# Kernel tuning notes

Hardware: AMD Instinct MI355X
Metric: run time of the kernel (lower is better)

Reference implementation:

```python
import jax, jax.numpy as jnp
import numpy as np
import math

D_MODEL = 768
N_HEADS = 12
D_HEAD = D_MODEL // N_HEADS


def setup_inputs() -> dict:
    key = jax.random.key(0)
    ks = jax.random.split(key, 5)
    x = jax.random.normal(ks[0], (2, 4096, D_MODEL), dtype=jnp.float32)
    s = 1.0 / math.sqrt(D_MODEL)
    W_qkv = jax.random.normal(ks[1], (D_MODEL, 3 * D_MODEL), dtype=jnp.float32) * s
    b_qkv = jnp.zeros((3 * D_MODEL,), dtype=jnp.float32)
    W_out = jax.random.normal(ks[2], (D_MODEL, D_MODEL), dtype=jnp.float32) * s
    b_out = jnp.zeros((D_MODEL,), dtype=jnp.float32)
    return {"x": x, "W_qkv": W_qkv, "b_qkv": b_qkv, "W_out": W_out, "b_out": b_out}


def reference(x, W_qkv, b_qkv, W_out, b_out):
    B, T, C = x.shape
    H, Dh = N_HEADS, D_HEAD
    qkv = x @ W_qkv + b_qkv                      # [B,T,3C]
    q, k, v = jnp.split(qkv, 3, axis=-1)
    q = q.reshape(B, T, H, Dh).transpose(0, 2, 1, 3)  # [B,H,T,Dh]
    k = k.reshape(B, T, H, Dh).transpose(0, 2, 1, 3)
    v = v.reshape(B, T, H, Dh).transpose(0, 2, 1, 3)
    att = jnp.einsum('bhqd,bhkd->bhqk', q, k) * (1.0 / math.sqrt(Dh))
    causal = jnp.tril(jnp.ones((T, T), dtype=bool))
    att = jnp.where(causal, att, -jnp.inf)
    att = jax.nn.softmax(att, axis=-1)
    out = jnp.einsum('bhqk,bhkd->bhqd', att, v)  # [B,H,T,Dh]
    out = out.transpose(0, 2, 1, 3).reshape(B, T, C)
    return out @ W_out + b_out
```

## Files before the change

### kernel.cpp

```cpp
#include <hip/hip_runtime.h>
#include <hip/hip_bf16.h>
#include <cstdint>

#define NH 12
#define DH 64
#define TSEQ 4096
#define BATCH 2
#define CDIM 768
#define MROWS (BATCH*TSEQ)

typedef __bf16 bf16x8 __attribute__((ext_vector_type(8)));
typedef __bf16 bf16x4 __attribute__((ext_vector_type(4)));
typedef bf16x8 bf16x8_a __attribute__((may_alias));
typedef bf16x4 bf16x4_a __attribute__((may_alias));
typedef float f32x4 __attribute__((ext_vector_type(4)));

__device__ __forceinline__ uint16_t f2bu(float f) {
  uint32_t u = __float_as_uint(f);
  u += 0x7fffu + ((u >> 16) & 1u);
  return (uint16_t)(u >> 16);
}

__device__ __forceinline__ float bu2f(uint16_t x) {
  return __uint_as_float(((uint32_t)x) << 16);
}

__device__ __forceinline__ void gload_lds16(const void* g, void* l) {
  __builtin_amdgcn_global_load_lds(
      (const __attribute__((address_space(1))) void*)g,
      (__attribute__((address_space(3))) void*)l, 16, 0, 0);
}

__global__ void cast_f32_bf16(const float* __restrict__ in, uint16_t* __restrict__ out, int n4) {
  int i = blockIdx.x * blockDim.x + threadIdx.x;
  int stride = gridDim.x * blockDim.x;
  for (; i < n4; i += stride) {
    float4 v = ((const float4*)in)[i];
    ushort4 o;
    o.x = f2bu(v.x); o.y = f2bu(v.y); o.z = f2bu(v.z); o.w = f2bu(v.w);
    ((ushort4*)out)[i] = o;
  }
}

__global__ void transpose_cast(const float* __restrict__ w, uint16_t* __restrict__ wt, int K, int N) {
  __shared__ float tile[32][33];
  int kb = blockIdx.x * 32, nb = blockIdx.y * 32;
  int tx = threadIdx.x & 31, ty = threadIdx.x >> 5;
  #pragma unroll
  for (int r = ty; r < 32; r += 8) tile[r][tx] = w[(size_t)(kb + r) * N + nb + tx];
  __syncthreads();
  #pragma unroll
  for (int r = ty; r < 32; r += 8) wt[(size_t)(nb + r) * K + kb + tx] = f2bu(tile[tx][r]);
}

template <int MODE>
__global__ __launch_bounds__(256) void gemm_bt(
    const uint16_t* __restrict__ A, const uint16_t* __restrict__ Bt,
    const float* __restrict__ bias,
    uint16_t* __restrict__ q, uint16_t* __restrict__ k, uint16_t* __restrict__ v,
    float* __restrict__ outf, int N, int K) {
  __shared__ uint16_t As[128 * 32];
  __shared__ uint16_t Bs[128 * 32];
  int tid = threadIdx.x;
  int w = tid >> 6, l = tid & 63;
  int lg = l >> 4, lr = l & 15;
  int mb = blockIdx.x * 128, nb = blockIdx.y * 128;
  int wr = (w >> 1) * 64, wc = (w & 1) * 64;
  f32x4 acc[4][4] = {};
  int srow = tid >> 2, scol = (tid & 3) * 8;
  const uint16_t* Ag = A + (size_t)(mb + srow) * K + scol;
  const uint16_t* Bg = Bt + (size_t)(nb + srow) * K + scol;
  char* AsB = (char*)As + (size_t)w * 1024;
  char* BsB = (char*)Bs + (size_t)w * 1024;
  size_t rowskip = (size_t)64 * K;
  for (int kb = 0; kb < K; kb += 32) {
    __syncthreads();
    gload_lds16(Ag + kb, AsB);
    gload_lds16(Ag + kb + rowskip, AsB + 4096);
    gload_lds16(Bg + kb, BsB);
    gload_lds16(Bg + kb + rowskip, BsB + 4096);
    __syncthreads();
    bf16x8 af[4], bfr[4];
    #pragma unroll
    for (int i = 0; i < 4; ++i)
      af[i] = *(const bf16x8_a*)(const void*)(As + (wr + i * 16 + lr) * 32 + lg * 8);
    #pragma unroll
    for (int i = 0; i < 4; ++i)
      bfr[i] = *(const bf16x8_a*)(const void*)(Bs + (wc + i * 16 + lr) * 32 + lg * 8);
    #pragma unroll
    for (int mi = 0; mi < 4; ++mi)
      #pragma unroll
      for (int ni = 0; ni < 4; ++ni)
        acc[mi][ni] = __builtin_amdgcn_mfma_f32_16x16x32_bf16(af[mi], bfr[ni], acc[mi][ni], 0, 0, 0);
  }
  #pragma unroll
  for (int mi = 0; mi < 4; ++mi) {
    #pragma unroll
    for (int ni = 0; ni < 4; ++ni) {
      if (MODE == 0) {
        int gm0 = mb + wr + mi * 16 + lg * 4;
        int gn = nb + wc + ni * 16 + lr;
        int which = gn / CDIM;
        int cc = gn - which * CDIM;
        int hh = cc >> 6, d = cc & 63;
        float bs = bias[gn];
        if (which == 2) {
          int b0 = gm0 >> 12, t0 = gm0 & 4095;
          ushort4 pk;
          pk.x = f2bu(acc[mi][ni][0] + bs);
          pk.y = f2bu(acc[mi][ni][1] + bs);
          pk.z = f2bu(acc[mi][ni][2] + bs);
          pk.w = f2bu(acc[mi][ni][3] + bs);
          *(ushort4*)&v[(((size_t)(b0 * NH + hh)) * DH + d) * TSEQ + t0] = pk;
        } else {
          uint16_t* dst = which ? k : q;
          float sc = which ? 1.0f : 0.1803368801111204f;
          #pragma unroll
          for (int j = 0; j < 4; ++j) {
            int gm = gm0 + j;
            int bb = gm >> 12, t = gm & 4095;
            float val = (acc[mi][ni][j] + bs) * sc;
            dst[(((size_t)(bb * NH + hh)) * TSEQ + t) * DH + d] = f2bu(val);
          }
        }
      } else {
        #pragma unroll
        for (int j = 0; j < 4; ++j) {
          int gm = mb + wr + mi * 16 + lg * 4 + j;
          int gn = nb + wc + ni * 16 + lr;
          outf[(size_t)gm * N + gn] = acc[mi][ni][j] + bias[gn];
        }
      }
    }
  }
}

__device__ __forceinline__ void tile_step(
    const uint16_t* __restrict__ Kc, const uint16_t* __restrict__ Vc, char* pw,
    bf16x8 qf0, bf16x8 qf1, f32x4 (&oacc)[4], float& lsum,
    bool diag, int thr, int lg, int lr, int swzA, int swzB) {
  f32x4 sacc[4];
  __builtin_amdgcn_s_setprio(1);
  #pragma unroll
  for (int ni = 0; ni < 4; ++ni) {
    const char* kb = (const char*)Kc + (ni * 16 + lr) * 128;
    bf16x8 kf0 = *(const bf16x8_a*)(kb + swzA);
    bf16x8 kf1 = *(const bf16x8_a*)(kb + swzB);
    f32x4 s = {};
    s = __builtin_amdgcn_mfma_f32_16x16x32_bf16(kf0, qf0, s, 0, 0, 0);
    s = __builtin_amdgcn_mfma_f32_16x16x32_bf16(kf1, qf1, s, 0, 0, 0);
    sacc[ni] = s;
  }
  __builtin_amdgcn_s_setprio(0);
  if (diag) {
    #pragma unroll
    for (int ni = 0; ni < 4; ++ni)
      #pragma unroll
      for (int j = 0; j < 4; ++j)
        sacc[ni][j] = (16 * ni + j <= thr) ? sacc[ni][j] : -1e30f;
  }
  int pofs = (lg & 1) * 8;
  #pragma unroll
  for (int ni = 0; ni < 4; ++ni) {
    float p0 = __builtin_amdgcn_exp2f(sacc[ni][0]);
    float p1 = __builtin_amdgcn_exp2f(sacc[ni][1]);
    float p2 = __builtin_amdgcn_exp2f(sacc[ni][2]);
    float p3 = __builtin_amdgcn_exp2f(sacc[ni][3]);
    lsum += (p0 + p1) + (p2 + p3);
    bf16x4 pk;
    pk[0] = (__bf16)p0; pk[1] = (__bf16)p1; pk[2] = (__bf16)p2; pk[3] = (__bf16)p3;
    int chunk = (2 * ni + (lg >> 1)) ^ (lr & 7);
    *(bf16x4_a*)(pw + lr * 128 + chunk * 16 + pofs) = pk;
  }
  bf16x8 pf0 = *(const bf16x8_a*)(pw + lr * 128 + swzA);
  bf16x8 pf1 = *(const bf16x8_a*)(pw + lr * 128 + swzB);
  __builtin_amdgcn_s_setprio(1);
  #pragma unroll
  for (int nd = 0; nd < 4; ++nd) {
    const char* vb = (const char*)Vc + (nd * 16 + lr) * 128;
    bf16x8 vf0 = *(const bf16x8_a*)(vb + swzA);
    bf16x8 vf1 = *(const bf16x8_a*)(vb + swzB);
    oacc[nd] = __builtin_amdgcn_mfma_f32_16x16x32_bf16(pf0, vf0, oacc[nd], 0, 0, 0);
    oacc[nd] = __builtin_amdgcn_mfma_f32_16x16x32_bf16(pf1, vf1, oacc[nd], 0, 0, 0);
  }
  __builtin_amdgcn_s_setprio(0);
}

__global__ __launch_bounds__(256) void attn_part(
    const uint16_t* __restrict__ Q, const uint16_t* __restrict__ K,
    const uint16_t* __restrict__ Vt, uint16_t* __restrict__ O,
    uint16_t* __restrict__ Pbuf, float* __restrict__ Plsum) {
  int gid = blockIdx.x;
  int widx = gid / 24, bh = gid - widx * 24;
  int qt, t0, t1, chunk;
  bool direct;
  if (widx < 32) {
    qt = 31 - (widx >> 1); chunk = widx & 1; direct = false;
    t0 = chunk ? (qt + 1) : 0;
    t1 = chunk ? (2 * qt + 1) : qt;
  } else {
    qt = 47 - widx; chunk = 0; direct = true;
    t0 = 0; t1 = 2 * qt + 1;
  }
  int b = bh / NH, hd = bh - b * NH;
  size_t base = (size_t)bh * TSEQ * DH;
  int tid = threadIdx.x, w = tid >> 6, lane = tid & 63;
  int lg = lane >> 4, lr = lane & 15;
  __shared__ uint16_t Ks[64 * 64];
  __shared__ uint16_t Vs[64 * 64];
  __shared__ uint16_t Ps[4][16 * 64];
  char* pw = (char*)Ps[w];
  int srow = tid >> 3;
  int schunk = (tid & 7) ^ (srow & 7);
  const uint16_t* Kg0 = K + base + (size_t)srow * DH + schunk * 8;
  const uint16_t* Vg0 = Vt + base + (size_t)srow * TSEQ + schunk * 8;
  char* KsB = (char*)Ks + w * 1024;
  char* VsB = (char*)Vs + w * 1024;
  int swzA = (lg ^ (lr & 7)) << 4;
  int swzB = swzA ^ 64;

  int qb = qt * 128;
  int qgA = qb + w * 16 + lr;
  int qgB = qgA + 64;
  bf16x8 qA0 = *(const bf16x8_a*)(const void*)(Q + base + (size_t)qgA * DH + lg * 8);
  bf16x8 qA1 = *(const bf16x8_a*)(const void*)(Q + base + (size_t)qgA * DH + 32 + lg * 8);
  bf16x8 qB0 = *(const bf16x8_a*)(const void*)(Q + base + (size_t)qgB * DH + lg * 8);
  bf16x8 qB1 = *(const bf16x8_a*)(const void*)(Q + base + (size_t)qgB * DH + 32 + lg * 8);
  f32x4 oA[4] = {}, oB[4] = {};
  float lA = 0.f, lB = 0.f;
  int lg4 = lg * 4;

  for (int t = t0; t <= t1; ++t) {
    __syncthreads();
    gload_lds16(Kg0 + (size_t)t * (64 * DH), KsB);
    gload_lds16(Kg0 + (size_t)t * (64 * DH) + 32 * DH, KsB + 4096);
    gload_lds16(Vg0 + (size_t)t * 64, VsB);
    gload_lds16(Vg0 + (size_t)t * 64 + (size_t)32 * TSEQ, VsB + 4096);
    __syncthreads();
    int kb0 = t * 64;
    if (t <= 2 * qt)
      tile_step(Ks, Vs, pw, qA0, qA1, oA, lA, t == 2 * qt, qgA - kb0 - lg4, lg, lr, swzA, swzB);
    tile_step(Ks, Vs, pw, qB0, qB1, oB, lB, t == 2 * qt + 1, qgB - kb0 - lg4, lg, lr, swzA, swzB);
  }

  lA += __shfl_xor(lA, 16, 64); lA += __shfl_xor(lA, 32, 64);
  lB += __shfl_xor(lB, 16, 64); lB += __shfl_xor(lB, 32, 64);
  if (direct) {
    float riA = 1.0f / lA, riB = 1.0f / lB;
    #pragma unroll
    for (int j = 0; j < 4; ++j) {
      float rvA = __shfl(riA, (lane & 48) | (lg4 + j), 64);
      float rvB = __shfl(riB, (lane & 48) | (lg4 + j), 64);
      int tA = qb + w * 16 + lg4 + j;
      size_t pA = (size_t)(b * TSEQ + tA) * CDIM + hd * DH + lr;
      size_t pB = pA + (size_t)64 * CDIM;
      #pragma unroll
      for (int nd = 0; nd < 4; ++nd) {
        O[pA + nd * 16] = f2bu(oA[nd][j] * rvA);
        O[pB + nd * 16] = f2bu(oB[nd][j] * rvB);
      }
    }
  } else {
    int pidx = (bh << 4) + (qt - 16);
    uint16_t* Pb = Pbuf + ((size_t)pidx * 2 + chunk) * 8192;
    float* Pl = Plsum + ((size_t)pidx * 2 + chunk) * 128;
    #pragma unroll
    for (int j = 0; j < 4; ++j) {
      int qlA = w * 16 + lg4 + j;
      #pragma unroll
      for (int nd = 0; nd < 4; ++nd) {
        Pb[qlA * 64 + nd * 16 + lr] = f2bu(oA[nd][j]);
        Pb[(64 + qlA) * 64 + nd * 16 + lr] = f2bu(oB[nd][j]);
      }
    }
    if (lane < 16) {
      Pl[w * 16 + lane] = lA;
      Pl[64 + w * 16 + lane] = lB;
    }
  }
}

__global__ __launch_bounds__(256) void attn_reduce(
    const uint16_t* __restrict__ Pbuf, const float* __restrict__ Plsum,
    uint16_t* __restrict__ O) {
  int pidx = blockIdx.x;
  int bh = pidx >> 4, qrel = pidx & 15;
  int qt = 16 + qrel;
  int b = bh / NH, hd = bh - b * NH;
  int d = threadIdx.x & 63, qo = threadIdx.x >> 6;
  const uint16_t* p0 = Pbuf + (size_t)pidx * 2 * 8192;
  const uint16_t* p1 = p0 + 8192;
  const float* l0 = Plsum + (size_t)pidx * 2 * 128;
  const float* l1 = l0 + 128;
  #pragma unroll 4
  for (int q = qo; q < 128; q += 4) {
    float li = 1.0f / (l0[q] + l1[q]);
    float s = bu2f(p0[q * 64 + d]) + bu2f(p1[q * 64 + d]);
    int t = qt * 128 + q;
    O[(size_t)(b * TSEQ + t) * CDIM + hd * DH + d] = f2bu(s * li);
  }
}

extern "C" void kernel_launch(void* const* d_in, const int* in_sizes, int n_in,
                              void* d_out, int out_size, void* d_ws, size_t ws_size,
                              hipStream_t stream) {
  const float* x    = (const float*)d_in[0];
  const float* Wqkv = (const float*)d_in[1];
  const float* bqkv = (const float*)d_in[2];
  const float* Wout = (const float*)d_in[3];
  const float* bout = (const float*)d_in[4];
  float* out = (float*)d_out;
  char* ws = (char*)d_ws;

  uint16_t* Xb    = (uint16_t*)(ws + 0);
  uint16_t* Wqkvt = (uint16_t*)(ws + 12582912);
  uint16_t* Woutt = (uint16_t*)(ws + 16121856);
  uint16_t* Qb    = (uint16_t*)(ws + 17301504);
  uint16_t* Kb    = (uint16_t*)(ws + 29884416);
  uint16_t* Vtb   = (uint16_t*)(ws + 42467328);
  uint16_t* Ob    = (uint16_t*)(ws + 55050240);
  uint16_t* Pbuf  = Xb;
  float*    Plsum = (float*)Wqkvt;

  cast_f32_bf16<<<2048, 256, 0, stream>>>(x, Xb, (MROWS * CDIM) / 4);
  transpose_cast<<<dim3(24, 72), 256, 0, stream>>>(Wqkv, Wqkvt, 768, 2304);
  transpose_cast<<<dim3(24, 24), 256, 0, stream>>>(Wout, Woutt, 768, 768);
  gemm_bt<0><<<dim3(64, 18), 256, 0, stream>>>(Xb, Wqkvt, bqkv, Qb, Kb, Vtb, nullptr, 2304, 768);
  attn_part<<<1152, 256, 0, stream>>>(Qb, Kb, Vtb, Ob, Pbuf, Plsum);
  attn_reduce<<<384, 256, 0, stream>>>(Pbuf, Plsum, Ob);
  gemm_bt<1><<<dim3(64, 6), 256, 0, stream>>>(Ob, Woutt, bout, nullptr, nullptr, nullptr, out, 768, 768);
}
```

Before: 196.9 us.

## Double-buffer K/V tiles and interleave both query blocks per tile

Allocates two LDS buffers for K and V and prefetches the next key tile while computing the current one, removing one barrier per iteration. It also fuses the two query-block tile steps so each K and V fragment read from LDS feeds MFMAs for both blocks. This doubles K/V LDS usage, raises register pressure, and depends on the async loads being complete by the single barrier.

```diff
diff --git a/kernel.cpp b/kernel.cpp
--- a/kernel.cpp
+++ b/kernel.cpp
@@ -135,57 +135,6 @@
   }
 }
 
-__device__ __forceinline__ void tile_step(
-    const uint16_t* __restrict__ Kc, const uint16_t* __restrict__ Vc, char* pw,
-    bf16x8 qf0, bf16x8 qf1, f32x4 (&oacc)[4], float& lsum,
-    bool diag, int thr, int lg, int lr, int swzA, int swzB) {
-  f32x4 sacc[4];
-  __builtin_amdgcn_s_setprio(1);
-  #pragma unroll
-  for (int ni = 0; ni < 4; ++ni) {
-    const char* kb = (const char*)Kc + (ni * 16 + lr) * 128;
-    bf16x8 kf0 = *(const bf16x8_a*)(kb + swzA);
-    bf16x8 kf1 = *(const bf16x8_a*)(kb + swzB);
-    f32x4 s = {};
-    s = __builtin_amdgcn_mfma_f32_16x16x32_bf16(kf0, qf0, s, 0, 0, 0);
-    s = __builtin_amdgcn_mfma_f32_16x16x32_bf16(kf1, qf1, s, 0, 0, 0);
-    sacc[ni] = s;
-  }
-  __builtin_amdgcn_s_setprio(0);
-  if (diag) {
-    #pragma unroll
-    for (int ni = 0; ni < 4; ++ni)
-      #pragma unroll
-      for (int j = 0; j < 4; ++j)
-        sacc[ni][j] = (16 * ni + j <= thr) ? sacc[ni][j] : -1e30f;
-  }
-  int pofs = (lg & 1) * 8;
-  #pragma unroll
-  for (int ni = 0; ni < 4; ++ni) {
-    float p0 = __builtin_amdgcn_exp2f(sacc[ni][0]);
-    float p1 = __builtin_amdgcn_exp2f(sacc[ni][1]);
-    float p2 = __builtin_amdgcn_exp2f(sacc[ni][2]);
-    float p3 = __builtin_amdgcn_exp2f(sacc[ni][3]);
-    lsum += (p0 + p1) + (p2 + p3);
-    bf16x4 pk;
-    pk[0] = (__bf16)p0; pk[1] = (__bf16)p1; pk[2] = (__bf16)p2; pk[3] = (__bf16)p3;
-    int chunk = (2 * ni + (lg >> 1)) ^ (lr & 7);
-    *(bf16x4_a*)(pw + lr * 128 + chunk * 16 + pofs) = pk;
-  }
-  bf16x8 pf0 = *(const bf16x8_a*)(pw + lr * 128 + swzA);
-  bf16x8 pf1 = *(const bf16x8_a*)(pw + lr * 128 + swzB);
-  __builtin_amdgcn_s_setprio(1);
-  #pragma unroll
-  for (int nd = 0; nd < 4; ++nd) {
-    const char* vb = (const char*)Vc + (nd * 16 + lr) * 128;
-    bf16x8 vf0 = *(const bf16x8_a*)(vb + swzA);
-    bf16x8 vf1 = *(const bf16x8_a*)(vb + swzB);
-    oacc[nd] = __builtin_amdgcn_mfma_f32_16x16x32_bf16(pf0, vf0, oacc[nd], 0, 0, 0);
-    oacc[nd] = __builtin_amdgcn_mfma_f32_16x16x32_bf16(pf1, vf1, oacc[nd], 0, 0, 0);
-  }
-  __builtin_amdgcn_s_setprio(0);
-}
-
 __global__ __launch_bounds__(256) void attn_part(
     const uint16_t* __restrict__ Q, const uint16_t* __restrict__ K,
     const uint16_t* __restrict__ Vt, uint16_t* __restrict__ O,
@@ -206,16 +155,14 @@
   size_t base = (size_t)bh * TSEQ * DH;
   int tid = threadIdx.x, w = tid >> 6, lane = tid & 63;
   int lg = lane >> 4, lr = lane & 15;
-  __shared__ uint16_t Ks[64 * 64];
-  __shared__ uint16_t Vs[64 * 64];
+  __shared__ __align__(16) uint16_t Ks[2][64 * 64];
+  __shared__ __align__(16) uint16_t Vs[2][64 * 64];
   __shared__ uint16_t Ps[4][16 * 64];
   char* pw = (char*)Ps[w];
   int srow = tid >> 3;
   int schunk = (tid & 7) ^ (srow & 7);
   const uint16_t* Kg0 = K + base + (size_t)srow * DH + schunk * 8;
   const uint16_t* Vg0 = Vt + base + (size_t)srow * TSEQ + schunk * 8;
-  char* KsB = (char*)Ks + w * 1024;
-  char* VsB = (char*)Vs + w * 1024;
   int swzA = (lg ^ (lr & 7)) << 4;
   int swzB = swzA ^ 64;
 
@@ -229,19 +176,114 @@
   f32x4 oA[4] = {}, oB[4] = {};
   float lA = 0.f, lB = 0.f;
   int lg4 = lg * 4;
-
+  int pofs = (lg & 1) * 8;
+
+#define STAGE(bufi, tv) do { \
+    char* kd_ = (char*)Ks[bufi] + w * 1024; \
+    char* vd_ = (char*)Vs[bufi] + w * 1024; \
+    const uint16_t* kg_ = Kg0 + (size_t)(tv) * (64 * DH); \
+    const uint16_t* vg_ = Vg0 + (size_t)(tv) * 64; \
+    gload_lds16(kg_,           kd_); \
+    gload_lds16(kg_ + 32 * DH, kd_ + 4096); \
+    gload_lds16(vg_,                     vd_); \
+    gload_lds16(vg_ + (size_t)32 * TSEQ, vd_ + 4096); \
+  } while (0)
+
+  STAGE(0, t0);
+  __syncthreads();
+  int cur = 0;
   for (int t = t0; t <= t1; ++t) {
+    if (t + 1 <= t1) STAGE(cur ^ 1, t + 1);
+    const uint16_t* Kc = Ks[cur];
+    const uint16_t* Vc = Vs[cur];
+    bool doA = (t <= 2 * qt);
+    int kb0 = t * 64;
+    f32x4 sA[4], sB[4];
+    __builtin_amdgcn_s_setprio(1);
+    #pragma unroll
+    for (int ni = 0; ni < 4; ++ni) {
+      const char* kbp = (const char*)Kc + (ni * 16 + lr) * 128;
+      bf16x8 kf0 = *(const bf16x8_a*)(kbp + swzA);
+      bf16x8 kf1 = *(const bf16x8_a*)(kbp + swzB);
+      f32x4 s = {};
+      s = __builtin_amdgcn_mfma_f32_16x16x32_bf16(kf0, qB0, s, 0, 0, 0);
+      s = __builtin_amdgcn_mfma_f32_16x16x32_bf16(kf1, qB1, s, 0, 0, 0);
+      sB[ni] = s;
+      if (doA) {
+        f32x4 sa = {};
+        sa = __builtin_amdgcn_mfma_f32_16x16x32_bf16(kf0, qA0, sa, 0, 0, 0);
+        sa = __builtin_amdgcn_mfma_f32_16x16x32_bf16(kf1, qA1, sa, 0, 0, 0);
+        sA[ni] = sa;
+      }
+    }
+    __builtin_amdgcn_s_setprio(0);
+    bf16x8 pfA0, pfA1;
+    if (doA) {
+      if (t == 2 * qt) {
+        int thr = qgA - kb0 - lg4;
+        #pragma unroll
+        for (int ni = 0; ni < 4; ++ni)
+          #pragma unroll
+          for (int j = 0; j < 4; ++j)
+            sA[ni][j] = (16 * ni + j <= thr) ? sA[ni][j] : -1e30f;
+      }
+      #pragma unroll
+      for (int ni = 0; ni < 4; ++ni) {
+        float p0 = __builtin_amdgcn_exp2f(sA[ni][0]);
+        float p1 = __builtin_amdgcn_exp2f(sA[ni][1]);
+        float p2 = __builtin_amdgcn_exp2f(sA[ni][2]);
+        float p3 = __builtin_amdgcn_exp2f(sA[ni][3]);
+        lA += (p0 + p1) + (p2 + p3);
+        bf16x4 pk;
+        pk[0] = (__bf16)p0; pk[1] = (__bf16)p1; pk[2] = (__bf16)p2; pk[3] = (__bf16)p3;
+        int chunkc = (2 * ni + (lg >> 1)) ^ (lr & 7);
+        *(bf16x4_a*)(pw + lr * 128 + chunkc * 16 + pofs) = pk;
+      }
+      pfA0 = *(const bf16x8_a*)(pw + lr * 128 + swzA);
+      pfA1 = *(const bf16x8_a*)(pw + lr * 128 + swzB);
+    }
+    {
+      if (t == 2 * qt + 1) {
+        int thr = qgB - kb0 - lg4;
+        #pragma unroll
+        for (int ni = 0; ni < 4; ++ni)
+          #pragma unroll
+          for (int j = 0; j < 4; ++j)
+            sB[ni][j] = (16 * ni + j <= thr) ? sB[ni][j] : -1e30f;
+      }
+      #pragma unroll
+      for (int ni = 0; ni < 4; ++ni) {
+        float p0 = __builtin_amdgcn_exp2f(sB[ni][0]);
+        float p1 = __builtin_amdgcn_exp2f(sB[ni][1]);
+        float p2 = __builtin_amdgcn_exp2f(sB[ni][2]);
+        float p3 = __builtin_amdgcn_exp2f(sB[ni][3]);
+        lB += (p0 + p1) + (p2 + p3);
+        bf16x4 pk;
+        pk[0] = (__bf16)p0; pk[1] = (__bf16)p1; pk[2] = (__bf16)p2; pk[3] = (__bf16)p3;
+        int chunkc = (2 * ni + (lg >> 1)) ^ (lr & 7);
+        *(bf16x4_a*)(pw + lr * 128 + chunkc * 16 + pofs) = pk;
+      }
+    }
+    bf16x8 pfB0 = *(const bf16x8_a*)(pw + lr * 128 + swzA);
+    bf16x8 pfB1 = *(const bf16x8_a*)(pw + lr * 128 + swzB);
+    __builtin_amdgcn_s_setprio(1);
+    #pragma unroll
+    for (int nd = 0; nd < 4; ++nd) {
+      const char* vb = (const char*)Vc + (nd * 16 + lr) * 128;
+      bf16x8 vf0 = *(const bf16x8_a*)(vb + swzA);
+      bf16x8 vf1 = *(const bf16x8_a*)(vb + swzB);
+      oB[nd] = __builtin_amdgcn_mfma_f32_16x16x32_bf16(pfB0, vf0, oB[nd], 0, 0, 0);
+      oB[nd] = __builtin_amdgcn_mfma_f32_16x16x32_bf16(pfB1, vf1, oB[nd], 0, 0, 0);
+      if (doA) {
+        oA[nd] = __builtin_amdgcn_mfma_f32_16x16x32_bf16(pfA0, vf0, oA[nd], 0, 0, 0);
+        oA[nd] = __builtin_amdgcn_mfma_f32_16x16x32_bf16(pfA1, vf1, oA[nd], 0, 0, 0);
+      }
+    }
+    __builtin_amdgcn_s_setprio(0);
     __syncthreads();
-    gload_lds16(Kg0 + (size_t)t * (64 * DH), KsB);
-    gload_lds16(Kg0 + (size_t)t * (64 * DH) + 32 * DH, KsB + 4096);
-    gload_lds16(Vg0 + (size_t)t * 64, VsB);
-    gload_lds16(Vg0 + (size_t)t * 64 + (size_t)32 * TSEQ, VsB + 4096);
-    __syncthreads();
-    int kb0 = t * 64;
-    if (t <= 2 * qt)
-      tile_step(Ks, Vs, pw, qA0, qA1, oA, lA, t == 2 * qt, qgA - kb0 - lg4, lg, lr, swzA, swzB);
-    tile_step(Ks, Vs, pw, qB0, qB1, oB, lB, t == 2 * qt + 1, qgB - kb0 - lg4, lg, lr, swzA, swzB);
-  }
+    cur ^= 1;
+  }
+#undef STAGE
 
   lA += __shfl_xor(lA, 16, 64); lA += __shfl_xor(lA, 32, 64);
   lB += __shfl_xor(lB, 16, 64); lB += __shfl_xor(lB, 32, 64);
```

After: 194.9 us. No clear change (-1.0%).
